# Kernel tuning notes

Measured on AMD Instinct MI355X. Metric: run time of the kernel, lower is better.

Reference implementation:

```python
import jax, jax.numpy as jnp
import numpy as np
import math

B, S, D, H, F, L = 16, 512, 1024, 16, 4096, 4
DK = D // H
NEG = -1e32


def _cosine_pe(max_len, d_model):
    # deterministic sin/cos table (the 0.1*randn init is fully overwritten for even d_model)
    pos = np.arange(max_len, dtype=np.float32)[:, None]
    div = np.exp(np.arange(0, d_model, 2, dtype=np.float32) * (-(math.log(10000.0) / d_model)))
    pe = np.zeros((max_len, d_model), dtype=np.float32)
    pe[:, 0::2] = np.sin(pos * div)
    pe[:, 1::2] = np.cos(pos * div)
    return jnp.asarray(pe)[None]  # [1, max_len, D]


def setup_inputs() -> dict:
    key = jax.random.key(0)
    ks = jax.random.split(key, 16)
    sc_d = 1.0 / math.sqrt(D)
    sc_f = 1.0 / math.sqrt(F)
    return {
        "q_embed_data": jax.random.normal(ks[0], (B, S, D), jnp.float32),
        "qa_embed_data": jax.random.normal(ks[1], (B, S, D), jnp.float32),
        "pe": _cosine_pe(S, D),
        "Wk": jax.random.normal(ks[2], (L, D, D), jnp.float32) * sc_d,
        "bk": jnp.zeros((L, D), jnp.float32),
        "Wv": jax.random.normal(ks[3], (L, D, D), jnp.float32) * sc_d,
        "bv": jnp.zeros((L, D), jnp.float32),
        "Wo": jax.random.normal(ks[4], (L, D, D), jnp.float32) * sc_d,
        "bo": jnp.zeros((L, D), jnp.float32),
        "ln1_g": jnp.ones((L, D), jnp.float32),
        "ln1_b": jnp.zeros((L, D), jnp.float32),
        "W1": jax.random.normal(ks[5], (L, D, F), jnp.float32) * sc_d,
        "b1": jnp.zeros((L, F), jnp.float32),
        "W2": jax.random.normal(ks[6], (L, F, D), jnp.float32) * sc_f,
        "b2": jnp.zeros((L, D), jnp.float32),
        "ln2_g": jnp.ones((L, D), jnp.float32),
        "ln2_b": jnp.zeros((L, D), jnp.float32),
    }


def _layer_norm(x, g, b, eps=1e-5):
    mu = jnp.mean(x, axis=-1, keepdims=True)
    var = jnp.var(x, axis=-1, keepdims=True)
    return (x - mu) * jax.lax.rsqrt(var + eps) * g + b


def _forward(q_embed_data, qa_embed_data, pe, Wk, bk, Wv, bv, Wo, bo,
             ln1_g, ln1_b, W1, b1, W2, b2, ln2_g, ln2_b):
    x = q_embed_data + pe[:, :S, :]
    y = qa_embed_data + pe[:, :S, :]  # values stay fixed across blocks
    # mask=0 in TransformerLayer: triu(k=0)==0 -> strictly-lower-triangular allowed
    allowed = jnp.tril(jnp.ones((S, S), bool), k=-1)  # [S, S]
    row_keep = (jnp.arange(S) > 0).astype(x.dtype)[None, None, :, None]  # zero_pad row 0
    scale = 1.0 / math.sqrt(DK)
    for l in range(L):
        # kq_same: q and k both use k_linear
        qk = (x @ Wk[l] + bk[l]).reshape(B, S, H, DK).transpose(0, 2, 1, 3)  # [B,H,S,DK]
        v = (y @ Wv[l] + bv[l]).reshape(B, S, H, DK).transpose(0, 2, 1, 3)
        scores = jnp.einsum('bhqd,bhkd->bhqk', qk, qk) * scale
        scores = jnp.where(allowed, scores, NEG)
        attn = jax.nn.softmax(scores, axis=-1) * row_keep  # zero_pad: first query row -> zeros
        ctx = jnp.einsum('bhqk,bhkd->bhqd', attn, v)
        ctx = ctx.transpose(0, 2, 1, 3).reshape(B, S, D)
        x = _layer_norm(x + (ctx @ Wo[l] + bo[l]), ln1_g[l], ln1_b[l])
        ffn = jax.nn.relu(x @ W1[l] + b1[l]) @ W2[l] + b2[l]
        x = _layer_norm(x + ffn, ln2_g[l], ln2_b[l])
    return x


def reference(q_embed_data, qa_embed_data, pe, Wk, bk, Wv, bv, Wo, bo,
              ln1_g, ln1_b, W1, b1, W2, b2, ln2_g, ln2_b):
    return _forward(q_embed_data, qa_embed_data, pe, Wk, bk, Wv, bv, Wo, bo,
                    ln1_g, ln1_b, W1, b1, W2, b2, ln2_g, ln2_b)
```

## Files before the change

### kernel.cpp

```cpp
#include <hip/hip_runtime.h>
#include <stdint.h>

typedef unsigned short u16;
typedef __bf16 bf16x8 __attribute__((ext_vector_type(8)));
typedef float f32x4 __attribute__((ext_vector_type(4)));

#define BDIM 16
#define SLEN 512
#define DMODEL 1024
#define NHEAD 16
#define DHEAD 64
#define FDIM 4096
#define NLAYER 4
#define ROWS (BDIM*SLEN)
#define KVT 64

__device__ __forceinline__ u16 f2b(float f) {
  uint32_t u = __builtin_bit_cast(uint32_t, f);
  u = (u + 0x7fffu + ((u >> 16) & 1u)) >> 16;
  return (u16)u;
}
__device__ __forceinline__ float b2f(u16 u) {
  return __builtin_bit_cast(float, (uint32_t)u << 16);
}
__device__ __forceinline__ float b2f_lo(uint32_t u) {
  return __builtin_bit_cast(float, u << 16);
}
__device__ __forceinline__ float b2f_hi(uint32_t u) {
  return __builtin_bit_cast(float, u & 0xffff0000u);
}

__device__ __forceinline__ void gl_lds16(const void* g, void* l) {
  uint32_t loff = (uint32_t)(uintptr_t)l;
  __builtin_amdgcn_global_load_lds(
      (__attribute__((address_space(1))) uint32_t*)(uintptr_t)g,
      (__attribute__((address_space(3))) uint32_t*)loff,
      16, 0, 0);
}

__global__ __launch_bounds__(256) void prep_kernel(const float4* __restrict__ q,
                                                   const float4* __restrict__ qa,
                                                   const float4* __restrict__ pe,
                                                   u16* __restrict__ xb,
                                                   u16* __restrict__ yb) {
  int idx = blockIdx.x * 256 + threadIdx.x;
  int pidx = idx & (SLEN * DMODEL / 4 - 1);
  float4 qv = q[idx], av = qa[idx], pv = pe[pidx];
  uint32_t x0 = (uint32_t)f2b(qv.x + pv.x) | ((uint32_t)f2b(qv.y + pv.y) << 16);
  uint32_t x1 = (uint32_t)f2b(qv.z + pv.z) | ((uint32_t)f2b(qv.w + pv.w) << 16);
  uint32_t y0 = (uint32_t)f2b(av.x + pv.x) | ((uint32_t)f2b(av.y + pv.y) << 16);
  uint32_t y1 = (uint32_t)f2b(av.z + pv.z) | ((uint32_t)f2b(av.w + pv.w) << 16);
  ((uint2*)xb)[idx] = make_uint2(x0, x1);
  ((uint2*)yb)[idx] = make_uint2(y0, y1);
}

__global__ __launch_bounds__(256) void transpose_f2b(const float* __restrict__ in,
                                                     u16* __restrict__ out,
                                                     int M, int N) {
  __shared__ float t[32][33];
  int tx = threadIdx.x & 31, ty = threadIdx.x >> 5;
  int m0 = blockIdx.y * 32, n0 = blockIdx.x * 32;
  const float* inz = in + (size_t)blockIdx.z * M * N;
  u16* outz = out + (size_t)blockIdx.z * M * N;
  #pragma unroll
  for (int i = 0; i < 32; i += 8) t[ty + i][tx] = inz[(size_t)(m0 + ty + i) * N + n0 + tx];
  __syncthreads();
  #pragma unroll
  for (int i = 0; i < 32; i += 8) outz[(size_t)(n0 + ty + i) * M + m0 + tx] = f2b(t[tx][ty + i]);
}

template<int BN, bool RELU, bool BF16OUT>
__global__ __launch_bounds__(512, 2) void gemm8p(const u16* __restrict__ Ap,
                                                 const u16* __restrict__ Bp,
                                                 const float* __restrict__ bias,
                                                 void* __restrict__ Cp,
                                                 int M, int N, int K) {
  constexpr int NBH = BN / 128;
  constexpr int NREP = BN / 64;
  constexpr int QN = NREP / 2;
  constexpr int HU = 8192;
  __shared__ __attribute__((aligned(16))) u16 lds[2][(2 + NBH) * HU];

  const int tid = threadIdx.x, wave = tid >> 6, lane = tid & 63;
  const int lg = lane >> 4, lc = lane & 15;
  const int wm = wave >> 2, wn = wave & 3;

  const int gx = gridDim.x;
  int nwg = gx * gridDim.y;
  int orig = blockIdx.y * gx + blockIdx.x;
  int qq = nwg >> 3, rr_ = nwg & 7;
  int xcd = orig & 7, ix = orig >> 3;
  int wg = (xcd < rr_ ? xcd * (qq + 1) : rr_ * (qq + 1) + (xcd - rr_) * qq) + ix;
  const int m0 = (wg / gx) * 256, n0 = (wg % gx) * BN;

  const int ldbyte = K * 2;
  const char* Ag = (const char*)Ap + (size_t)m0 * ldbyte;
  const char* Bg = (const char*)Bp + (size_t)n0 * ldbyte;

  int o1 = tid * 16, o2 = 8192 + tid * 16;
  int sr1 = o1 >> 7, sg1 = (((o1 >> 4) & 7) - sr1) & 7;
  int sr2 = o2 >> 7, sg2 = (((o2 >> 4) & 7) - sr2) & 7;
  const int soff1 = sr1 * ldbyte + sg1 * 16;
  const int soff2 = sr2 * ldbyte + sg2 * 16;
  const int NT = K >> 6;

  auto stageA = [&](int kt, int h, int buf) {
    const char* g = Ag + (size_t)h * 128 * ldbyte + (size_t)kt * 128;
    char* d = (char*)&lds[buf][h * HU] + wave * 1024;
    gl_lds16(g + soff1, d);
    gl_lds16(g + soff2, d + 8192);
  };
  auto stageB = [&](int kt, int h, int buf) {
    const char* g = Bg + (size_t)h * 128 * ldbyte + (size_t)kt * 128;
    char* d = (char*)&lds[buf][(2 + h) * HU] + wave * 1024;
    gl_lds16(g + soff1, d);
    gl_lds16(g + soff2, d + 8192);
  };

  const int bstart = wn * (BN / 4);
  const int bh = bstart >> 7, bc0 = bstart & 127;

  auto rdA = [&](const u16* base, int f, int kk) -> bf16x8 {
    int row = f * 16 + lc;
    return *(const bf16x8*)&base[row * 64 + (((kk * 4 + lg + row) & 7) << 3)];
  };
  auto rdB = [&](const u16* base, int jj, int kk) -> bf16x8 {
    int row = bc0 + jj * 16 + lc;
    return *(const bf16x8*)&base[row * 64 + (((kk * 4 + lg + row) & 7) << 3)];
  };

  f32x4 acc[8][NREP];
  #pragma unroll
  for (int f = 0; f < 8; f++)
    #pragma unroll
    for (int j = 0; j < NREP; j++) acc[f][j] = (f32x4){0.f, 0.f, 0.f, 0.f};

  stageA(0, 0, 0); stageA(0, 1, 0);
  stageB(0, 0, 0); if (NBH == 2) stageB(0, 1, 0);
  stageA(1, 0, 1); stageA(1, 1, 1);
  asm volatile("s_waitcnt vmcnt(4)\n\ts_barrier" ::: "memory");

  auto ktile = [&](int k, int buf) {
    const u16* Ab_ = &lds[buf][wm * HU];
    const u16* Bb_ = &lds[buf][(2 + bh) * HU];
    const int kn = (k + 1 < NT) ? k + 1 : NT - 1;
    const int k2 = (k + 2 < NT) ? k + 2 : NT - 1;
    bf16x8 a0[4][2], a1[4][2], b0[QN][2], b1[QN][2];

    #pragma unroll
    for (int f = 0; f < 4; f++) { a0[f][0] = rdA(Ab_, f, 0); a0[f][1] = rdA(Ab_, f, 1); }
    #pragma unroll
    for (int j = 0; j < QN; j++) { b0[j][0] = rdB(Bb_, j, 0); b0[j][1] = rdB(Bb_, j, 1); }
    stageB(kn, 0, buf ^ 1);
    asm volatile("s_barrier" ::: "memory");
    __builtin_amdgcn_s_setprio(1);
    #pragma unroll
    for (int f = 0; f < 4; f++)
      #pragma unroll
      for (int j = 0; j < QN; j++) {
        acc[f][j] = __builtin_amdgcn_mfma_f32_16x16x32_bf16(a0[f][0], b0[j][0], acc[f][j], 0, 0, 0);
        acc[f][j] = __builtin_amdgcn_mfma_f32_16x16x32_bf16(a0[f][1], b0[j][1], acc[f][j], 0, 0, 0);
      }
    __builtin_amdgcn_s_setprio(0);
    asm volatile("s_barrier" ::: "memory");

    #pragma unroll
    for (int f = 0; f < 4; f++) { a1[f][0] = rdA(Ab_, 4 + f, 0); a1[f][1] = rdA(Ab_, 4 + f, 1); }
    if (NBH == 2) stageB(kn, 1, buf ^ 1);
    asm volatile("s_barrier" ::: "memory");
    __builtin_amdgcn_s_setprio(1);
    #pragma unroll
    for (int f = 0; f < 4; f++)
      #pragma unroll
      for (int j = 0; j < QN; j++) {
        acc[4 + f][j] = __builtin_amdgcn_mfma_f32_16x16x32_bf16(a1[f][0], b0[j][0], acc[4 + f][j], 0, 0, 0);
        acc[4 + f][j] = __builtin_amdgcn_mfma_f32_16x16x32_bf16(a1[f][1], b0[j][1], acc[4 + f][j], 0, 0, 0);
      }
    __builtin_amdgcn_s_setprio(0);
    asm volatile("s_barrier" ::: "memory");

    #pragma unroll
    for (int j = 0; j < QN; j++) { b1[j][0] = rdB(Bb_, QN + j, 0); b1[j][1] = rdB(Bb_, QN + j, 1); }
    stageA(k2, 0, buf);
    asm volatile("s_barrier" ::: "memory");
    __builtin_amdgcn_s_setprio(1);
    #pragma unroll
    for (int f = 0; f < 4; f++)
      #pragma unroll
      for (int j = 0; j < QN; j++) {
        acc[4 + f][QN + j] = __builtin_amdgcn_mfma_f32_16x16x32_bf16(a1[f][0], b1[j][0], acc[4 + f][QN + j], 0, 0, 0);
        acc[4 + f][QN + j] = __builtin_amdgcn_mfma_f32_16x16x32_bf16(a1[f][1], b1[j][1], acc[4 + f][QN + j], 0, 0, 0);
      }
    __builtin_amdgcn_s_setprio(0);
    asm volatile("s_barrier" ::: "memory");

    stageA(k2, 1, buf);
    asm volatile("s_barrier" ::: "memory");
    __builtin_amdgcn_s_setprio(1);
    #pragma unroll
    for (int f = 0; f < 4; f++)
      #pragma unroll
      for (int j = 0; j < QN; j++) {
        acc[f][QN + j] = __builtin_amdgcn_mfma_f32_16x16x32_bf16(a0[f][0], b1[j][0], acc[f][QN + j], 0, 0, 0);
        acc[f][QN + j] = __builtin_amdgcn_mfma_f32_16x16x32_bf16(a0[f][1], b1[j][1], acc[f][QN + j], 0, 0, 0);
      }
    __builtin_amdgcn_s_setprio(0);
    asm volatile("s_waitcnt vmcnt(4)\n\ts_barrier" ::: "memory");
  };

  for (int k = 0; k < NT; k += 2) {
    ktile(k, 0);
    ktile(k + 1, 1);
  }

  #pragma unroll
  for (int f = 0; f < 8; f++) {
    int row = m0 + wm * 128 + f * 16 + lg * 4;
    #pragma unroll
    for (int j = 0; j < NREP; j++) {
      int col = n0 + bstart + j * 16 + lc;
      float bv = bias[col];
      #pragma unroll
      for (int t2 = 0; t2 < 4; t2++) {
        float v = acc[f][j][t2] + bv;
        if (RELU) v = fmaxf(v, 0.f);
        if (BF16OUT) ((u16*)Cp)[(size_t)(row + t2) * N + col] = f2b(v);
        else         ((float*)Cp)[(size_t)(row + t2) * N + col] = v;
      }
    }
  }
}

template<bool RESID>
__global__ __launch_bounds__(256, 2) void gemm4w(const u16* __restrict__ Ap,
                                                 const u16* __restrict__ Bp,
                                                 const float* __restrict__ bias,
                                                 const u16* __restrict__ Rp,
                                                 u16* __restrict__ Cp,
                                                 int M, int N, int K) {
  __shared__ __attribute__((aligned(16))) u16 As[2][128 * 64];
  __shared__ __attribute__((aligned(16))) u16 Bs[2][128 * 64];
  const int tid = threadIdx.x, wave = tid >> 6, lane = tid & 63;
  const int lg = lane >> 4, lc = lane & 15;
  const int wm = wave >> 1, wn = wave & 1;

  const int gx = gridDim.x;
  int nwg = gx * gridDim.y;
  int orig = blockIdx.y * gx + blockIdx.x;
  int qq = nwg >> 3, rr_ = nwg & 7;
  int xcd = orig & 7, ix = orig >> 3;
  int wg = (xcd < rr_ ? xcd * (qq + 1) : rr_ * (qq + 1) + (xcd - rr_) * qq) + ix;
  const int m0 = (wg / gx) * 128, n0 = (wg % gx) * 128;

  const int ldbyte = K * 2;
  const char* Ag = (const char*)Ap + (size_t)m0 * ldbyte;
  const char* Bg = (const char*)Bp + (size_t)n0 * ldbyte;
  const int NT = K >> 6;

  auto stage = [&](const char* gb, int kt, u16* lb) {
    #pragma unroll
    for (int c = 0; c < 4; c++) {
      int o = c * 4096 + tid * 16;
      int row = o >> 7;
      int g = (((o >> 4) & 7) - row) & 7;
      gl_lds16(gb + (size_t)row * ldbyte + (size_t)kt * 128 + g * 16,
               (char*)lb + c * 4096 + wave * 1024);
    }
  };
  auto rd = [&](const u16* base, int strip, int f, int kk) -> bf16x8 {
    int row = strip * 64 + f * 16 + lc;
    return *(const bf16x8*)&base[row * 64 + (((kk * 4 + lg + row) & 7) << 3)];
  };

  f32x4 acc[4][4];
  #pragma unroll
  for (int f = 0; f < 4; f++)
    #pragma unroll
    for (int n = 0; n < 4; n++) acc[f][n] = (f32x4){0.f, 0.f, 0.f, 0.f};

  stage(Ag, 0, As[0]); stage(Bg, 0, Bs[0]);
  stage(Ag, 1, As[1]); stage(Bg, 1, Bs[1]);
  asm volatile("s_waitcnt vmcnt(8)\n\ts_barrier" ::: "memory");

  for (int k = 0; k < NT; k++) {
    const int buf = k & 1;
    const int k2 = (k + 2 < NT) ? k + 2 : k;
    bf16x8 a[4][2], b[4][2];
    #pragma unroll
    for (int f = 0; f < 4; f++) { a[f][0] = rd(As[buf], wm, f, 0); a[f][1] = rd(As[buf], wm, f, 1); }
    #pragma unroll
    for (int n = 0; n < 4; n++) { b[n][0] = rd(Bs[buf], wn, n, 0); b[n][1] = rd(Bs[buf], wn, n, 1); }
    asm volatile("s_barrier" ::: "memory");
    __builtin_amdgcn_s_setprio(1);
    #pragma unroll
    for (int f = 0; f < 4; f++)
      #pragma unroll
      for (int n = 0; n < 2; n++) {
        acc[f][n] = __builtin_amdgcn_mfma_f32_16x16x32_bf16(a[f][0], b[n][0], acc[f][n], 0, 0, 0);
        acc[f][n] = __builtin_amdgcn_mfma_f32_16x16x32_bf16(a[f][1], b[n][1], acc[f][n], 0, 0, 0);
      }
    __builtin_amdgcn_s_setprio(0);
    asm volatile("s_waitcnt lgkmcnt(0)\n\ts_barrier" ::: "memory");
    stage(Ag, k2, As[buf]);
    stage(Bg, k2, Bs[buf]);
    __builtin_amdgcn_s_setprio(1);
    #pragma unroll
    for (int f = 0; f < 4; f++)
      #pragma unroll
      for (int n = 2; n < 4; n++) {
        acc[f][n] = __builtin_amdgcn_mfma_f32_16x16x32_bf16(a[f][0], b[n][0], acc[f][n], 0, 0, 0);
        acc[f][n] = __builtin_amdgcn_mfma_f32_16x16x32_bf16(a[f][1], b[n][1], acc[f][n], 0, 0, 0);
      }
    __builtin_amdgcn_s_setprio(0);
    asm volatile("s_waitcnt vmcnt(8)\n\ts_barrier" ::: "memory");
  }

  #pragma unroll
  for (int f = 0; f < 4; f++) {
    int row = m0 + wm * 64 + f * 16 + lg * 4;
    #pragma unroll
    for (int n = 0; n < 4; n++) {
      int col = n0 + wn * 64 + n * 16 + lc;
      float bv = bias[col];
      #pragma unroll
      for (int r = 0; r < 4; r++) {
        float v = acc[f][n][r] + bv;
        if (RESID) v += b2f(Rp[(size_t)(row + r) * N + col]);
        Cp[(size_t)(row + r) * N + col] = f2b(v);
      }
    }
  }
}

__global__ __launch_bounds__(256, 4) void attn_kernel(const u16* __restrict__ QK,
                                                      const u16* __restrict__ V,
                                                      u16* __restrict__ CTX) {
  __shared__ __attribute__((aligned(16))) u16 Ks[2][KVT * 64];
  __shared__ __attribute__((aligned(16))) u16 VTs[64 * 72];
  __shared__ __attribute__((aligned(16))) u16 Ps[4][16 * 72];
  const int qt = blockIdx.x, bh = blockIdx.y;
  const int b = bh >> 4, h = bh & 15;
  const char* Qg = (const char*)(QK + (size_t)b * SLEN * DMODEL + h * DHEAD);
  const char* Vg = (const char*)(V + (size_t)b * SLEN * DMODEL + h * DHEAD);
  const int tid = threadIdx.x, wave = tid >> 6, lane = tid & 63;
  const int lg = lane >> 4, lc = lane & 15;
  const int ktmax = qt;

  auto stageK = [&](int kt, int buf) {
    #pragma unroll
    for (int i = 0; i < 2; i++) {
      int o = i * 4096 + tid * 16;
      int row = o >> 7, slot = (o >> 4) & 7;
      int g = (slot - row) & 7;
      gl_lds16(Qg + (size_t)(kt * KVT + row) * (DMODEL * 2) + g * 16,
               (char*)Ks[buf] + i * 4096 + wave * 1024);
    }
  };
  const int vhi = lane >> 5, vls = lane & 31;
  const int vc_ = wave + 4 * vhi;
  auto loadV = [&](int kt, uint4 (&va)[2]) {
    const char* src = Vg + (size_t)(kt * KVT + 2 * vls) * (DMODEL * 2) + vc_ * 16;
    va[0] = *(const uint4*)src;
    va[1] = *(const uint4*)(src + DMODEL * 2);
  };
  auto writeVT = [&](const uint4 (&va)[2]) {
    u16 e0[8], e1[8];
    *(uint4*)e0 = va[0];
    *(uint4*)e1 = va[1];
    #pragma unroll
    for (int j = 0; j < 8; j++) {
      uint32_t pk = (uint32_t)e0[j] | ((uint32_t)e1[j] << 16);
      *(uint32_t*)&VTs[(8 * vc_ + j) * 72 + 2 * vls] = pk;
    }
  };

  uint4 vaA[2], vaB[2];
  const int qrow = qt * 64 + wave * 16 + lc;
  bf16x8 aq0 = *(const bf16x8*)(Qg + (size_t)qrow * (DMODEL * 2) + lg * 16);
  bf16x8 aq1 = *(const bf16x8*)(Qg + (size_t)qrow * (DMODEL * 2) + 64 + lg * 16);
  stageK(0, 0);
  loadV(0, vaA);
  stageK(ktmax > 0 ? 1 : 0, 1);
  asm volatile("s_waitcnt vmcnt(2)\n\ts_barrier" ::: "memory");

  float l_run[4] = {0.f, 0.f, 0.f, 0.f};
  f32x4 acc_o[4];
  #pragma unroll
  for (int n = 0; n < 4; n++) acc_o[n] = (f32x4){0.f, 0.f, 0.f, 0.f};

  auto iter = [&](int kt, int cur, uint4 (&vc)[2], uint4 (&vn)[2]) {
    const int kn = (kt + 1 <= ktmax) ? kt + 1 : ktmax;
    const int k2 = (kt + 2 <= ktmax) ? kt + 2 : kt;

    asm volatile("s_waitcnt vmcnt(2) lgkmcnt(0)" ::: "memory");
    __builtin_amdgcn_s_barrier();
    writeVT(vc);
    loadV(kn, vn);

    f32x4 sc[4];
    #pragma unroll
    for (int n = 0; n < 4; n++) sc[n] = (f32x4){0.f, 0.f, 0.f, 0.f};
    #pragma unroll
    for (int n = 0; n < 4; n++) {
      int row = n * 16 + lc;
      bf16x8 bk0 = *(const bf16x8*)&Ks[cur][row * 64 + (((lg + row) & 7) << 3)];
      bf16x8 bk1 = *(const bf16x8*)&Ks[cur][row * 64 + (((4 + lg + row) & 7) << 3)];
      sc[n] = __builtin_amdgcn_mfma_f32_16x16x32_bf16(aq0, bk0, sc[n], 0, 0, 0);
      sc[n] = __builtin_amdgcn_mfma_f32_16x16x32_bf16(aq1, bk1, sc[n], 0, 0, 0);
    }

    const int qbase = qt * 64 + wave * 16 + lg * 4;
    #pragma unroll
    for (int n = 0; n < 4; n++) {
      int kg = kt * KVT + n * 16 + lc;
      #pragma unroll
      for (int r = 0; r < 4; r++) {
        float e = __expf(fmaf(sc[n][r], 0.125f, -24.f));
        float p = (kg < qbase + r) ? e : 0.f;
        l_run[r] += p;
        Ps[wave][(lg * 4 + r) * 72 + n * 16 + lc] = f2b(p);
      }
    }

    asm volatile("s_waitcnt lgkmcnt(0)" ::: "memory");
    __builtin_amdgcn_s_barrier();
    stageK(k2, cur);

    bf16x8 ap0 = *(const bf16x8*)&Ps[wave][lc * 72 + lg * 8];
    bf16x8 ap1 = *(const bf16x8*)&Ps[wave][lc * 72 + 32 + lg * 8];
    #pragma unroll
    for (int n2 = 0; n2 < 4; n2++) {
      bf16x8 bv0 = *(const bf16x8*)&VTs[(n2 * 16 + lc) * 72 + lg * 8];
      bf16x8 bv1 = *(const bf16x8*)&VTs[(n2 * 16 + lc) * 72 + 32 + lg * 8];
      acc_o[n2] = __builtin_amdgcn_mfma_f32_16x16x32_bf16(ap0, bv0, acc_o[n2], 0, 0, 0);
      acc_o[n2] = __builtin_amdgcn_mfma_f32_16x16x32_bf16(ap1, bv1, acc_o[n2], 0, 0, 0);
    }
  };

  for (int kt = 0; kt <= ktmax; kt += 2) {
    iter(kt, 0, vaA, vaB);
    if (kt + 1 <= ktmax) iter(kt + 1, 1, vaB, vaA);
  }

  #pragma unroll
  for (int d = 1; d < 16; d <<= 1)
    #pragma unroll
    for (int r = 0; r < 4; r++) l_run[r] += __shfl_xor(l_run[r], d, 64);

  asm volatile("s_waitcnt vmcnt(0)" ::: "memory");
  #pragma unroll
  for (int n2 = 0; n2 < 4; n2++)
    #pragma unroll
    for (int r = 0; r < 4; r++) {
      int sq = qt * 64 + wave * 16 + lg * 4 + r;
      float v = (sq == 0) ? 0.f : acc_o[n2][r] / l_run[r];
      CTX[((size_t)b * SLEN + sq) * DMODEL + h * DHEAD + n2 * 16 + lc] = f2b(v);
    }
}

__global__ __launch_bounds__(256) void ln_kernel(const u16* __restrict__ tmp,
                                                 u16* __restrict__ xb,
                                                 const float* __restrict__ gw,
                                                 const float* __restrict__ bw) {
  __shared__ float red[4], red2[4];
  const int row = blockIdx.x, t = threadIdx.x;
  const size_t base = (size_t)row * DMODEL + t * 4;
  uint2 tv = *(const uint2*)&tmp[base];
  float v[4];
  v[0] = b2f_lo(tv.x); v[1] = b2f_hi(tv.x);
  v[2] = b2f_lo(tv.y); v[3] = b2f_hi(tv.y);
  float s = v[0] + v[1] + v[2] + v[3];
  #pragma unroll
  for (int d = 1; d < 64; d <<= 1) s += __shfl_xor(s, d, 64);
  if ((t & 63) == 0) red[t >> 6] = s;
  __syncthreads();
  float mean = (red[0] + red[1] + red[2] + red[3]) * (1.f / DMODEL);
  float q2 = 0.f;
  #pragma unroll
  for (int i = 0; i < 4; i++) { float d_ = v[i] - mean; q2 += d_ * d_; }
  #pragma unroll
  for (int d = 1; d < 64; d <<= 1) q2 += __shfl_xor(q2, d, 64);
  if ((t & 63) == 0) red2[t >> 6] = q2;
  __syncthreads();
  float var = (red2[0] + red2[1] + red2[2] + red2[3]) * (1.f / DMODEL);
  float rs = rsqrtf(var + 1e-5f);
  float4 gv = *(const float4*)&gw[t * 4];
  float4 bv4 = *(const float4*)&bw[t * 4];
  float o0 = (v[0] - mean) * rs * gv.x + bv4.x;
  float o1 = (v[1] - mean) * rs * gv.y + bv4.y;
  float o2 = (v[2] - mean) * rs * gv.z + bv4.z;
  float o3 = (v[3] - mean) * rs * gv.w + bv4.w;
  uint2 pk;
  pk.x = (uint32_t)f2b(o0) | ((uint32_t)f2b(o1) << 16);
  pk.y = (uint32_t)f2b(o2) | ((uint32_t)f2b(o3) << 16);
  *(uint2*)&xb[base] = pk;
}

__global__ __launch_bounds__(256) void expand_kernel(const uint2* __restrict__ src,
                                                     float4* __restrict__ dst) {
  int i = blockIdx.x * 256 + threadIdx.x;
  uint2 v = src[i];
  dst[i] = make_float4(b2f_lo(v.x), b2f_hi(v.x), b2f_lo(v.y), b2f_hi(v.y));
}

extern "C" void kernel_launch(void* const* d_in, const int* in_sizes, int n_in,
                              void* d_out, int out_size, void* d_ws, size_t ws_size,
                              hipStream_t stream) {
  (void)in_sizes; (void)n_in; (void)out_size;
  const float* q    = (const float*)d_in[0];
  const float* qa   = (const float*)d_in[1];
  const float* pe   = (const float*)d_in[2];
  const float* Wk   = (const float*)d_in[3];
  const float* bk   = (const float*)d_in[4];
  const float* Wv   = (const float*)d_in[5];
  const float* bv   = (const float*)d_in[6];
  const float* Wo   = (const float*)d_in[7];
  const float* bo   = (const float*)d_in[8];
  const float* ln1g = (const float*)d_in[9];
  const float* ln1b = (const float*)d_in[10];
  const float* W1   = (const float*)d_in[11];
  const float* b1   = (const float*)d_in[12];
  const float* W2   = (const float*)d_in[13];
  const float* b2   = (const float*)d_in[14];
  const float* ln2g = (const float*)d_in[15];
  const float* ln2b = (const float*)d_in[16];

  char* w = (char*)d_ws;
  u16* xb   = (u16*)w; w += (size_t)ROWS * DMODEL * 2;
  u16* yb   = (u16*)w; w += (size_t)ROWS * DMODEL * 2;
  u16* qkb  = (u16*)w; w += (size_t)ROWS * DMODEL * 2;
  u16* vb   = (u16*)w; w += (size_t)ROWS * DMODEL * 2;
  u16* ctxb = (u16*)w; w += (size_t)ROWS * DMODEL * 2;
  u16* ffnb = (u16*)w; w += (size_t)ROWS * FDIM * 2;
  u16* tmpb = qkb;

  const size_t DD = (size_t)DMODEL * DMODEL, DF = (size_t)DMODEL * FDIM;
  size_t used = (size_t)(w - (char*)d_ws);
  const bool hoist = ws_size >= used + (3 * DD + 2 * DF) * NLAYER * 2;

  u16 *WkT, *WvT, *WoT, *W1T, *W2T;
  if (hoist) {
    WkT = (u16*)w; w += DD * NLAYER * 2;
    WvT = (u16*)w; w += DD * NLAYER * 2;
    WoT = (u16*)w; w += DD * NLAYER * 2;
    W1T = (u16*)w; w += DF * NLAYER * 2;
    W2T = (u16*)w; w += DF * NLAYER * 2;
  } else {
    WkT = (u16*)w; w += DD * 2;
    WvT = (u16*)w; w += DD * 2;
    WoT = (u16*)w; w += DD * 2;
    W1T = (u16*)w; w += DF * 2;
    W2T = (u16*)w; w += DF * 2;
  }

  prep_kernel<<<ROWS * DMODEL / 4 / 256, 256, 0, stream>>>(
      (const float4*)q, (const float4*)qa, (const float4*)pe, xb, yb);

  if (hoist) {
    transpose_f2b<<<dim3(32, 32, NLAYER), 256, 0, stream>>>(Wk, WkT, DMODEL, DMODEL);
    transpose_f2b<<<dim3(32, 32, NLAYER), 256, 0, stream>>>(Wv, WvT, DMODEL, DMODEL);
    transpose_f2b<<<dim3(32, 32, NLAYER), 256, 0, stream>>>(Wo, WoT, DMODEL, DMODEL);
    transpose_f2b<<<dim3(128, 32, NLAYER), 256, 0, stream>>>(W1, W1T, DMODEL, FDIM);
    transpose_f2b<<<dim3(32, 128, NLAYER), 256, 0, stream>>>(W2, W2T, FDIM, DMODEL);
  }

  for (int l = 0; l < NLAYER; l++) {
    u16 *WkTl, *WvTl, *WoTl, *W1Tl, *W2Tl;
    if (hoist) {
      WkTl = WkT + l * DD; WvTl = WvT + l * DD; WoTl = WoT + l * DD;
      W1Tl = W1T + l * DF; W2Tl = W2T + l * DF;
    } else {
      transpose_f2b<<<dim3(32, 32), 256, 0, stream>>>(Wk + l * DD, WkT, DMODEL, DMODEL);
      transpose_f2b<<<dim3(32, 32), 256, 0, stream>>>(Wv + l * DD, WvT, DMODEL, DMODEL);
      transpose_f2b<<<dim3(32, 32), 256, 0, stream>>>(Wo + l * DD, WoT, DMODEL, DMODEL);
      transpose_f2b<<<dim3(128, 32), 256, 0, stream>>>(W1 + l * DF, W1T, DMODEL, FDIM);
      transpose_f2b<<<dim3(32, 128), 256, 0, stream>>>(W2 + l * DF, W2T, FDIM, DMODEL);
      WkTl = WkT; WvTl = WvT; WoTl = WoT; W1Tl = W1T; W2Tl = W2T;
    }

    gemm4w<false><<<dim3(DMODEL / 128, ROWS / 128), 256, 0, stream>>>(
        xb, WkTl, bk + l * DMODEL, nullptr, qkb, ROWS, DMODEL, DMODEL);
    gemm4w<false><<<dim3(DMODEL / 128, ROWS / 128), 256, 0, stream>>>(
        yb, WvTl, bv + l * DMODEL, nullptr, vb, ROWS, DMODEL, DMODEL);
    attn_kernel<<<dim3(SLEN / 64, BDIM * NHEAD), 256, 0, stream>>>(qkb, vb, ctxb);
    gemm4w<true><<<dim3(DMODEL / 128, ROWS / 128), 256, 0, stream>>>(
        ctxb, WoTl, bo + l * DMODEL, xb, tmpb, ROWS, DMODEL, DMODEL);
    ln_kernel<<<ROWS, 256, 0, stream>>>(tmpb, xb, ln1g + l * DMODEL, ln1b + l * DMODEL);
    gemm8p<256, true, true><<<dim3(FDIM / 256, ROWS / 256), 512, 0, stream>>>(
        xb, W1Tl, b1 + l * FDIM, ffnb, ROWS, FDIM, DMODEL);
    gemm4w<true><<<dim3(DMODEL / 128, ROWS / 128), 256, 0, stream>>>(
        ffnb, W2Tl, b2 + l * DMODEL, xb, tmpb, ROWS, DMODEL, FDIM);
    ln_kernel<<<ROWS, 256, 0, stream>>>(tmpb, xb, ln2g + l * DMODEL, ln2b + l * DMODEL);
  }
  expand_kernel<<<ROWS * DMODEL / 4 / 256, 256, 0, stream>>>((const uint2*)xb, (float4*)d_out);
}
```

Measured before the change: 1.177 ms.

## Double attention query tile per block and fuse final expand into LayerNorm

The attention kernel now processes 128 query rows per block, 32 per wave in two 16-row fragments, so each staged K/V tile feeds twice as many MFMAs. This halves the number of blocks and the repeated K/V loads, at the cost of more registers (launch bounds drop to 2 blocks per CU) and some wasted work on the fully masked diagonal tiles. Separately, the last LayerNorm writes fp32 output directly, removing the separate bf16-to-fp32 expand kernel and its extra pass over memory.

Measured after the change: 1.133 ms. -3.8%, faster.

```diff
diff --git a/kernel.cpp b/kernel.cpp
--- a/kernel.cpp
+++ b/kernel.cpp
@@ -14,6 +14,7 @@
 #define NLAYER 4
 #define ROWS (BDIM*SLEN)
 #define KVT 64
+#define QBLK 128
 
 __device__ __forceinline__ u16 f2b(float f) {
   uint32_t u = __builtin_bit_cast(uint32_t, f);
@@ -332,19 +333,19 @@
   }
 }
 
-__global__ __launch_bounds__(256, 4) void attn_kernel(const u16* __restrict__ QK,
+__global__ __launch_bounds__(256, 2) void attn_kernel(const u16* __restrict__ QK,
                                                       const u16* __restrict__ V,
                                                       u16* __restrict__ CTX) {
   __shared__ __attribute__((aligned(16))) u16 Ks[2][KVT * 64];
   __shared__ __attribute__((aligned(16))) u16 VTs[64 * 72];
-  __shared__ __attribute__((aligned(16))) u16 Ps[4][16 * 72];
+  __shared__ __attribute__((aligned(16))) u16 Ps[4][32 * 72];
   const int qt = blockIdx.x, bh = blockIdx.y;
   const int b = bh >> 4, h = bh & 15;
   const char* Qg = (const char*)(QK + (size_t)b * SLEN * DMODEL + h * DHEAD);
   const char* Vg = (const char*)(V + (size_t)b * SLEN * DMODEL + h * DHEAD);
   const int tid = threadIdx.x, wave = tid >> 6, lane = tid & 63;
   const int lg = lane >> 4, lc = lane & 15;
-  const int ktmax = qt;
+  const int ktmax = (qt * QBLK + QBLK - 2) >> 6;
 
   auto stageK = [&](int kt, int buf) {
     #pragma unroll
@@ -375,18 +376,24 @@
   };
 
   uint4 vaA[2], vaB[2];
-  const int qrow = qt * 64 + wave * 16 + lc;
-  bf16x8 aq0 = *(const bf16x8*)(Qg + (size_t)qrow * (DMODEL * 2) + lg * 16);
-  bf16x8 aq1 = *(const bf16x8*)(Qg + (size_t)qrow * (DMODEL * 2) + 64 + lg * 16);
+  bf16x8 aq[2][2];
+  #pragma unroll
+  for (int f = 0; f < 2; f++) {
+    const int qrow = qt * QBLK + wave * 32 + f * 16 + lc;
+    aq[f][0] = *(const bf16x8*)(Qg + (size_t)qrow * (DMODEL * 2) + lg * 16);
+    aq[f][1] = *(const bf16x8*)(Qg + (size_t)qrow * (DMODEL * 2) + 64 + lg * 16);
+  }
   stageK(0, 0);
   loadV(0, vaA);
-  stageK(ktmax > 0 ? 1 : 0, 1);
+  stageK(1, 1);
   asm volatile("s_waitcnt vmcnt(2)\n\ts_barrier" ::: "memory");
 
-  float l_run[4] = {0.f, 0.f, 0.f, 0.f};
-  f32x4 acc_o[4];
-  #pragma unroll
-  for (int n = 0; n < 4; n++) acc_o[n] = (f32x4){0.f, 0.f, 0.f, 0.f};
+  float l_run[2][4] = {{0.f, 0.f, 0.f, 0.f}, {0.f, 0.f, 0.f, 0.f}};
+  f32x4 acc_o[2][4];
+  #pragma unroll
+  for (int f = 0; f < 2; f++)
+    #pragma unroll
+    for (int n = 0; n < 4; n++) acc_o[f][n] = (f32x4){0.f, 0.f, 0.f, 0.f};
 
   auto iter = [&](int kt, int cur, uint4 (&vc)[2], uint4 (&vn)[2]) {
     const int kn = (kt + 1 <= ktmax) ? kt + 1 : ktmax;
@@ -397,28 +404,36 @@
     writeVT(vc);
     loadV(kn, vn);
 
-    f32x4 sc[4];
-    #pragma unroll
-    for (int n = 0; n < 4; n++) sc[n] = (f32x4){0.f, 0.f, 0.f, 0.f};
+    f32x4 sc[2][4];
+    #pragma unroll
+    for (int f = 0; f < 2; f++)
+      #pragma unroll
+      for (int n = 0; n < 4; n++) sc[f][n] = (f32x4){0.f, 0.f, 0.f, 0.f};
     #pragma unroll
     for (int n = 0; n < 4; n++) {
       int row = n * 16 + lc;
       bf16x8 bk0 = *(const bf16x8*)&Ks[cur][row * 64 + (((lg + row) & 7) << 3)];
       bf16x8 bk1 = *(const bf16x8*)&Ks[cur][row * 64 + (((4 + lg + row) & 7) << 3)];
-      sc[n] = __builtin_amdgcn_mfma_f32_16x16x32_bf16(aq0, bk0, sc[n], 0, 0, 0);
-      sc[n] = __builtin_amdgcn_mfma_f32_16x16x32_bf16(aq1, bk1, sc[n], 0, 0, 0);
-    }
-
-    const int qbase = qt * 64 + wave * 16 + lg * 4;
-    #pragma unroll
-    for (int n = 0; n < 4; n++) {
-      int kg = kt * KVT + n * 16 + lc;
-      #pragma unroll
-      for (int r = 0; r < 4; r++) {
-        float e = __expf(fmaf(sc[n][r], 0.125f, -24.f));
-        float p = (kg < qbase + r) ? e : 0.f;
-        l_run[r] += p;
-        Ps[wave][(lg * 4 + r) * 72 + n * 16 + lc] = f2b(p);
+      #pragma unroll
+      for (int f = 0; f < 2; f++) {
+        sc[f][n] = __builtin_amdgcn_mfma_f32_16x16x32_bf16(aq[f][0], bk0, sc[f][n], 0, 0, 0);
+        sc[f][n] = __builtin_amdgcn_mfma_f32_16x16x32_bf16(aq[f][1], bk1, sc[f][n], 0, 0, 0);
+      }
+    }
+
+    #pragma unroll
+    for (int f = 0; f < 2; f++) {
+      const int qbase = qt * QBLK + wave * 32 + f * 16 + lg * 4;
+      #pragma unroll
+      for (int n = 0; n < 4; n++) {
+        int kg = kt * KVT + n * 16 + lc;
+        #pragma unroll
+        for (int r = 0; r < 4; r++) {
+          float e = __expf(fmaf(sc[f][n][r], 0.125f, -24.f));
+          float p = (kg < qbase + r) ? e : 0.f;
+          l_run[f][r] += p;
+          Ps[wave][(f * 16 + lg * 4 + r) * 72 + n * 16 + lc] = f2b(p);
+        }
       }
     }
 
@@ -426,42 +441,55 @@
     __builtin_amdgcn_s_barrier();
     stageK(k2, cur);
 
-    bf16x8 ap0 = *(const bf16x8*)&Ps[wave][lc * 72 + lg * 8];
-    bf16x8 ap1 = *(const bf16x8*)&Ps[wave][lc * 72 + 32 + lg * 8];
+    bf16x8 ap[2][2];
+    #pragma unroll
+    for (int f = 0; f < 2; f++) {
+      ap[f][0] = *(const bf16x8*)&Ps[wave][(f * 16 + lc) * 72 + lg * 8];
+      ap[f][1] = *(const bf16x8*)&Ps[wave][(f * 16 + lc) * 72 + 32 + lg * 8];
+    }
     #pragma unroll
     for (int n2 = 0; n2 < 4; n2++) {
       bf16x8 bv0 = *(const bf16x8*)&VTs[(n2 * 16 + lc) * 72 + lg * 8];
       bf16x8 bv1 = *(const bf16x8*)&VTs[(n2 * 16 + lc) * 72 + 32 + lg * 8];
-      acc_o[n2] = __builtin_amdgcn_mfma_f32_16x16x32_bf16(ap0, bv0, acc_o[n2], 0, 0, 0);
-      acc_o[n2] = __builtin_amdgcn_mfma_f32_16x16x32_bf16(ap1, bv1, acc_o[n2], 0, 0, 0);
+      #pragma unroll
+      for (int f = 0; f < 2; f++) {
+        acc_o[f][n2] = __builtin_amdgcn_mfma_f32_16x16x32_bf16(ap[f][0], bv0, acc_o[f][n2], 0, 0, 0);
+        acc_o[f][n2] = __builtin_amdgcn_mfma_f32_16x16x32_bf16(ap[f][1], bv1, acc_o[f][n2], 0, 0, 0);
+      }
     }
   };
 
   for (int kt = 0; kt <= ktmax; kt += 2) {
     iter(kt, 0, vaA, vaB);
-    if (kt + 1 <= ktmax) iter(kt + 1, 1, vaB, vaA);
+    iter(kt + 1, 1, vaB, vaA);
   }
 
   #pragma unroll
   for (int d = 1; d < 16; d <<= 1)
     #pragma unroll
-    for (int r = 0; r < 4; r++) l_run[r] += __shfl_xor(l_run[r], d, 64);
+    for (int f = 0; f < 2; f++)
+      #pragma unroll
+      for (int r = 0; r < 4; r++) l_run[f][r] += __shfl_xor(l_run[f][r], d, 64);
 
   asm volatile("s_waitcnt vmcnt(0)" ::: "memory");
   #pragma unroll
-  for (int n2 = 0; n2 < 4; n2++)
-    #pragma unroll
-    for (int r = 0; r < 4; r++) {
-      int sq = qt * 64 + wave * 16 + lg * 4 + r;
-      float v = (sq == 0) ? 0.f : acc_o[n2][r] / l_run[r];
-      CTX[((size_t)b * SLEN + sq) * DMODEL + h * DHEAD + n2 * 16 + lc] = f2b(v);
-    }
-}
-
+  for (int f = 0; f < 2; f++)
+    #pragma unroll
+    for (int n2 = 0; n2 < 4; n2++)
+      #pragma unroll
+      for (int r = 0; r < 4; r++) {
+        int sq = qt * QBLK + wave * 32 + f * 16 + lg * 4 + r;
+        float v = (sq == 0) ? 0.f : acc_o[f][n2][r] / l_run[f][r];
+        CTX[((size_t)b * SLEN + sq) * DMODEL + h * DHEAD + n2 * 16 + lc] = f2b(v);
+      }
+}
+
+template<bool OUT32>
 __global__ __launch_bounds__(256) void ln_kernel(const u16* __restrict__ tmp,
                                                  u16* __restrict__ xb,
                                                  const float* __restrict__ gw,
-                                                 const float* __restrict__ bw) {
+                                                 const float* __restrict__ bw,
+                                                 float4* __restrict__ outf) {
   __shared__ float red[4], red2[4];
   const int row = blockIdx.x, t = threadIdx.x;
   const size_t base = (size_t)row * DMODEL + t * 4;
@@ -490,17 +518,15 @@
   float o1 = (v[1] - mean) * rs * gv.y + bv4.y;
   float o2 = (v[2] - mean) * rs * gv.z + bv4.z;
   float o3 = (v[3] - mean) * rs * gv.w + bv4.w;
-  uint2 pk;
-  pk.x = (uint32_t)f2b(o0) | ((uint32_t)f2b(o1) << 16);
-  pk.y = (uint32_t)f2b(o2) | ((uint32_t)f2b(o3) << 16);
-  *(uint2*)&xb[base] = pk;
-}
-
-__global__ __launch_bounds__(256) void expand_kernel(const uint2* __restrict__ src,
-                                                     float4* __restrict__ dst) {
-  int i = blockIdx.x * 256 + threadIdx.x;
-  uint2 v = src[i];
-  dst[i] = make_float4(b2f_lo(v.x), b2f_hi(v.x), b2f_lo(v.y), b2f_hi(v.y));
+  if (OUT32) {
+    outf[(size_t)row * (DMODEL / 4) + t] =
+        make_float4(b2f(f2b(o0)), b2f(f2b(o1)), b2f(f2b(o2)), b2f(f2b(o3)));
+  } else {
+    uint2 pk;
+    pk.x = (uint32_t)f2b(o0) | ((uint32_t)f2b(o1) << 16);
+    pk.y = (uint32_t)f2b(o2) | ((uint32_t)f2b(o3) << 16);
+    *(uint2*)&xb[base] = pk;
+  }
 }
 
 extern "C" void kernel_launch(void* const* d_in, const int* in_sizes, int n_in,
@@ -582,15 +608,19 @@
         xb, WkTl, bk + l * DMODEL, nullptr, qkb, ROWS, DMODEL, DMODEL);
     gemm4w<false><<<dim3(DMODEL / 128, ROWS / 128), 256, 0, stream>>>(
         yb, WvTl, bv + l * DMODEL, nullptr, vb, ROWS, DMODEL, DMODEL);
-    attn_kernel<<<dim3(SLEN / 64, BDIM * NHEAD), 256, 0, stream>>>(qkb, vb, ctxb);
+    attn_kernel<<<dim3(SLEN / QBLK, BDIM * NHEAD), 256, 0, stream>>>(qkb, vb, ctxb);
     gemm4w<true><<<dim3(DMODEL / 128, ROWS / 128), 256, 0, stream>>>(
         ctxb, WoTl, bo + l * DMODEL, xb, tmpb, ROWS, DMODEL, DMODEL);
-    ln_kernel<<<ROWS, 256, 0, stream>>>(tmpb, xb, ln1g + l * DMODEL, ln1b + l * DMODEL);
+    ln_kernel<false><<<ROWS, 256, 0, stream>>>(tmpb, xb, ln1g + l * DMODEL, ln1b + l * DMODEL, nullptr);
     gemm8p<256, true, true><<<dim3(FDIM / 256, ROWS / 256), 512, 0, stream>>>(
         xb, W1Tl, b1 + l * FDIM, ffnb, ROWS, FDIM, DMODEL);
     gemm4w<true><<<dim3(DMODEL / 128, ROWS / 128), 256, 0, stream>>>(
         ffnb, W2Tl, b2 + l * DMODEL, xb, tmpb, ROWS, DMODEL, FDIM);
-    ln_kernel<<<ROWS, 256, 0, stream>>>(tmpb, xb, ln2g + l * DMODEL, ln2b + l * DMODEL);
-  }
-  expand_kernel<<<ROWS * DMODEL / 4 / 256, 256, 0, stream>>>((const uint2*)xb, (float4*)d_out);
-}
+    if (l == NLAYER - 1) {
+      ln_kernel<true><<<ROWS, 256, 0, stream>>>(tmpb, xb, ln2g + l * DMODEL, ln2b + l * DMODEL,
+                                                (float4*)d_out);
+    } else {
+      ln_kernel<false><<<ROWS, 256, 0, stream>>>(tmpb, xb, ln2g + l * DMODEL, ln2b + l * DMODEL, nullptr);
+    }
+  }
+}
```
